# Optimization experiments

Hardware: AMD Instinct MI355X
Metric: run time of the kernel (lower is better)

Reference implementation:

```python
import jax, jax.numpy as jnp
import numpy as np

NUM_NODES = 32768  # B*N = 16*2048
NUM_REL = 10
NUM_BASES = 4
D = 256
E = 524288


def _rgcn_layer(x, src, dst, rel, basis, comp, root, bias):
    """Basis-decomposed relational GCN layer with per-relation mean aggregation.
    x: [N, Din], basis: [NB, Din, Dout], comp: [R, NB], root: [Din, Dout], bias: [Dout].
    """
    n = x.shape[0]
    # project all nodes through each basis once: [N, NB, Dout]
    xb = jnp.einsum('ni,bio->nbo', x, basis)
    coeff = comp[rel]  # [E, NB] per-edge basis coefficients
    # mean normalization per (destination node, relation) pair
    seg = rel * n + dst  # combined segment id, [E]
    cnt = jax.ops.segment_sum(jnp.ones(rel.shape[0], x.dtype), seg,
                              num_segments=NUM_REL * n)
    inv = jnp.where(cnt > 0, 1.0 / cnt, 0.0)[seg]  # [E]
    # per-edge message: sum_b coeff[e,b] * xb[src_e, b, :] (loop over small NB)
    msg = jnp.zeros((rel.shape[0], basis.shape[2]), x.dtype)
    for b in range(basis.shape[0]):
        msg = msg + coeff[:, b:b + 1] * xb[src, b]
    msg = msg * inv[:, None]
    agg = jax.ops.segment_sum(msg, dst, num_segments=n)  # [N, Dout]
    return agg + x @ root + bias


def setup_inputs() -> dict:
    key = jax.random.key(0)
    ks = jax.random.split(key, 16)
    p = lambda k, shp: (jax.random.normal(k, shp, jnp.float32) * 0.05)
    inp = {
        'x': jax.random.normal(ks[0], (16, 2048, D), jnp.float32),
        't': jax.random.randint(ks[1], (16,), 0, 1000),
        'obj_cond': jax.random.randint(ks[2], (16, 2048), 0, 160),
        'edge_cond': jax.random.randint(ks[3], (2, E), 0, NUM_NODES),
        'relation_cond': jax.random.randint(ks[4], (E,), 0, NUM_REL),
        # layer 0: 256 -> 256 (hidden)
        'basis0': p(ks[5], (NUM_BASES, D, D)),
        'comp0': p(ks[6], (NUM_REL, NUM_BASES)),
        'root0': p(ks[7], (D, D)),
        'bias0': p(ks[8], (D,)),
        # layer 1: 256 -> 256 (output)
        'basis1': p(ks[9], (NUM_BASES, D, D)),
        'comp1': p(ks[10], (NUM_REL, NUM_BASES)),
        'root1': p(ks[11], (D, D)),
        'bias1': p(ks[12], (D,)),
    }
    return inp


def reference(x, t, obj_cond, edge_cond, relation_cond,
              basis0, comp0, root0, bias0, basis1, comp1, root1, bias1):
    B, N, Dm = x.shape
    h = x.reshape(B * N, Dm)
    src, dst = edge_cond[0], edge_cond[1]
    h = _rgcn_layer(h, src, dst, relation_cond, basis0, comp0, root0, bias0)
    h = jax.nn.relu(h)  # hidden-layer activation (dropout disabled at eval)
    h = _rgcn_layer(h, src, dst, relation_cond, basis1, comp1, root1, bias1)
    return h.reshape(B, N, Dm)
```

## Files before the change

### kernel.cpp

```cpp
#include <hip/hip_runtime.h>
#include <stdint.h>

#define NNODES 32768
#define NREL 10
#define NBASES 4
#define DIM 256
#define NEDGE 524288
#define KW 1280
#define KBASE 1024

#define HB 2048
#define CB 8192
#define WB 80

typedef __attribute__((ext_vector_type(8))) short bf16x8;
typedef __attribute__((ext_vector_type(4))) float f32x4;

__device__ __forceinline__ float bf2f(unsigned short u){
  union { unsigned int i; float f; } v; v.i = ((unsigned int)u) << 16; return v.f;
}
__device__ __forceinline__ unsigned short f2bf(float f){
  union { float f; unsigned int i; } v; v.f = f;
  unsigned int x = v.i;
  unsigned int r = (x + 0x7FFFu + ((x >> 16) & 1u)) >> 16;
  return (unsigned short)r;
}
__device__ __forceinline__ void gll16(const void* g, void* l){
  __builtin_amdgcn_global_load_lds((const __attribute__((address_space(1))) void*)g,
                                   (__attribute__((address_space(3))) void*)l, 16, 0, 0);
}

__global__ __launch_bounds__(256) void mega_prep(
    const int* __restrict__ ec, const int* __restrict__ rel,
    int* __restrict__ cnt_rd,
    const float* __restrict__ x, unsigned short* __restrict__ Xh,
    const float* __restrict__ basis0, const float* __restrict__ root0,
    unsigned short* __restrict__ Wt0,
    const float* __restrict__ basis1, const float* __restrict__ root1,
    unsigned short* __restrict__ Wt1)
{
  __shared__ float tile[64][65];
  int bid = blockIdx.x;
  int t = threadIdx.x;
  if (bid < HB){
    int e = bid * 256 + t;
    int d = ec[NEDGE + e];
    int r = rel[e];
    atomicAdd(&cnt_rd[(r << 15) + d], 1);
  } else if (bid < HB + CB){
    int i = (bid - HB) * 256 + t;
    float4 v = ((const float4*)x)[i];
    ushort4 o; o.x = f2bf(v.x); o.y = f2bf(v.y); o.z = f2bf(v.z); o.w = f2bf(v.w);
    ((ushort4*)Xh)[i] = o;
  } else {
    int b = bid - HB - CB;
    int layer = b / WB; b %= WB;
    const float* basis = layer ? basis1 : basis0;
    const float* root  = layer ? root1  : root0;
    unsigned short* Wt = layer ? Wt1    : Wt0;
    int k0 = (b % 20) * 64;
    int n0 = (b / 20) * 64;
    int tn = t & 63, tk = t >> 6;
#pragma unroll
    for (int i = 0; i < 64; i += 4){
      int k = k0 + tk + i;
      float v = (k < KBASE) ? basis[(size_t)k * 256 + n0 + tn]
                            : root[(size_t)(k - KBASE) * 256 + n0 + tn];
      tile[tk + i][tn] = v;
    }
    __syncthreads();
#pragma unroll
    for (int i = 0; i < 64; i += 4){
      int n = n0 + tk + i;
      Wt[(size_t)n * KW + k0 + tn] = f2bf(tile[tn][tk + i]);
    }
  }
}

__global__ __launch_bounds__(1024) void scan1(const int* __restrict__ cnt_rd,
                                              int* __restrict__ offs, int* __restrict__ blksum)
{
  __shared__ int sh[1024];
  int tid = threadIdx.x; int gid = blockIdx.x * 1024 + tid;
  int v = 0;
#pragma unroll
  for (int r = 0; r < NREL; r++) v += cnt_rd[(r << 15) + gid];
  sh[tid] = v; __syncthreads();
  for (int off = 1; off < 1024; off <<= 1){
    int t = (tid >= off) ? sh[tid - off] : 0;
    __syncthreads(); sh[tid] += t; __syncthreads();
  }
  offs[gid] = sh[tid] - v;
  if (tid == 1023) blksum[blockIdx.x] = sh[1023];
}
__global__ __launch_bounds__(64) void scan2(int* __restrict__ blksum)
{
  __shared__ int sh[64];
  int tid = threadIdx.x;
  int v = (tid < NNODES / 1024) ? blksum[tid] : 0;
  sh[tid] = v; __syncthreads();
  for (int off = 1; off < 64; off <<= 1){
    int t = (tid >= off) ? sh[tid - off] : 0;
    __syncthreads(); sh[tid] += t; __syncthreads();
  }
  if (tid < NNODES / 1024) blksum[tid] = sh[tid] - v;
}
__global__ __launch_bounds__(1024) void scan3(int* __restrict__ offs, const int* __restrict__ blksum)
{
  int gid = blockIdx.x * 1024 + threadIdx.x;
  offs[gid] += blksum[blockIdx.x];
  if (gid == 0) offs[NNODES] = NEDGE;
}

__global__ void scatter_kernel(const int* __restrict__ ec, const int* __restrict__ rel,
                               const int* __restrict__ offs, int* __restrict__ cursor,
                               unsigned int* __restrict__ meta)
{
  int e = blockIdx.x * 256 + threadIdx.x;
  int s = ec[e];
  int d = ec[NEDGE + e];
  int r = rel[e];
  int p = offs[d] + atomicAdd(&cursor[d], 1);
  meta[p] = ((unsigned int)s << 4) | (unsigned int)r;
}

__global__ __launch_bounds__(256) void agg5(
    const unsigned short* __restrict__ Xin,
    const int* __restrict__ offs,
    const unsigned int* __restrict__ meta,
    const float* __restrict__ comp,
    const int* __restrict__ cnt_rd,
    unsigned short* __restrict__ z)
{
  __shared__ __attribute__((aligned(16))) float wtab[4][40];
  int t = threadIdx.x;
  int wv = t >> 6, lane = t & 63;
  int d = blockIdx.x * 4 + wv;
  if (lane < 40){
    int r = lane >> 2, b = lane & 3;
    int cnt = cnt_rd[(r << 15) + d];
    wtab[wv][lane] = (cnt > 0) ? comp[r * NBASES + b] / (float)cnt : 0.0f;
  }
  __syncthreads();

  int col = lane * 4;
  const float4* wt4 = (const float4*)&wtab[wv][0];

  float acc[NBASES][4] = {};
  int e0 = offs[d], e1 = offs[d + 1];
  int e = e0;
  for (; e + 3 < e1; e += 4){
    unsigned int m0 = meta[e], m1 = meta[e + 1], m2 = meta[e + 2], m3 = meta[e + 3];
    float4 w0 = wt4[m0 & 15u], w1 = wt4[m1 & 15u], w2 = wt4[m2 & 15u], w3 = wt4[m3 & 15u];
    ushort4 v0 = *(const ushort4*)(Xin + ((size_t)(m0 >> 4)) * 256 + col);
    ushort4 v1 = *(const ushort4*)(Xin + ((size_t)(m1 >> 4)) * 256 + col);
    ushort4 v2 = *(const ushort4*)(Xin + ((size_t)(m2 >> 4)) * 256 + col);
    ushort4 v3 = *(const ushort4*)(Xin + ((size_t)(m3 >> 4)) * 256 + col);
#pragma unroll
    for (int b = 0; b < NBASES; b++){
      float a0 = ((const float*)&w0)[b];
      float a1 = ((const float*)&w1)[b];
      float a2 = ((const float*)&w2)[b];
      float a3 = ((const float*)&w3)[b];
      acc[b][0] += a0 * bf2f(v0.x) + a1 * bf2f(v1.x) + a2 * bf2f(v2.x) + a3 * bf2f(v3.x);
      acc[b][1] += a0 * bf2f(v0.y) + a1 * bf2f(v1.y) + a2 * bf2f(v2.y) + a3 * bf2f(v3.y);
      acc[b][2] += a0 * bf2f(v0.z) + a1 * bf2f(v1.z) + a2 * bf2f(v2.z) + a3 * bf2f(v3.z);
      acc[b][3] += a0 * bf2f(v0.w) + a1 * bf2f(v1.w) + a2 * bf2f(v2.w) + a3 * bf2f(v3.w);
    }
  }
  for (; e < e1; ++e){
    unsigned int md = meta[e];
    float4 w = wt4[md & 15u];
    ushort4 v = *(const ushort4*)(Xin + ((size_t)(md >> 4)) * 256 + col);
#pragma unroll
    for (int b = 0; b < NBASES; b++){
      float a = ((const float*)&w)[b];
      acc[b][0] += a * bf2f(v.x); acc[b][1] += a * bf2f(v.y);
      acc[b][2] += a * bf2f(v.z); acc[b][3] += a * bf2f(v.w);
    }
  }
#pragma unroll
  for (int b = 0; b < NBASES; b++){
    ushort4 o;
    o.x = f2bf(acc[b][0]); o.y = f2bf(acc[b][1]);
    o.z = f2bf(acc[b][2]); o.w = f2bf(acc[b][3]);
    *(ushort4*)(z + (size_t)d * KBASE + b * 256 + col) = o;
  }
}

__global__ __launch_bounds__(256) void gemm4(
    const unsigned short* __restrict__ A0,
    const unsigned short* __restrict__ A1,
    const unsigned short* __restrict__ Wt,
    const float* __restrict__ bias,
    unsigned short* __restrict__ outh,
    float* __restrict__ outf,
    int mode)
{
  __shared__ __attribute__((aligned(16))) short As[64 * 32];
  __shared__ __attribute__((aligned(16))) short Bs[256 * 32];
  int tid  = threadIdx.x;
  int m0   = blockIdx.x * 64;
  int lane = tid & 63;
  int wn   = tid >> 6;
  int lq = lane >> 4, lr = lane & 15;

  f32x4 zero = {0.f, 0.f, 0.f, 0.f};
  f32x4 acc[4][4];
#pragma unroll
  for (int i = 0; i < 4; i++)
#pragma unroll
    for (int j = 0; j < 4; j++) acc[i][j] = zero;

  int arow = tid >> 2;
  int akc  = ((tid & 3) - (tid >> 3)) & 3;

  for (int k0 = 0; k0 < KW; k0 += 32){
    __syncthreads();
    {
      const unsigned short* ga;
      if (k0 < KBASE) ga = A0 + (size_t)(m0 + arow) * KBASE + k0 + akc * 8;
      else            ga = A1 + (size_t)(m0 + arow) * 256 + (k0 - KBASE) + akc * 8;
      gll16(ga, As + tid * 8);
    }
#pragma unroll
    for (int i = 0; i < 4; i++){
      int gb  = tid + i * 256;
      int row = gb >> 2;
      int kc  = ((gb & 3) - (gb >> 3)) & 3;
      gll16(Wt + (size_t)row * KW + k0 + kc * 8, Bs + gb * 8);
    }
    __syncthreads();

    bf16x8 af[4], bfr[4];
#pragma unroll
    for (int i = 0; i < 4; i++){
      int row = i * 16 + lr;
      af[i] = *(const bf16x8*)(As + row * 32 + (((lq + (row >> 1)) & 3) * 8));
    }
#pragma unroll
    for (int j = 0; j < 4; j++){
      int row = wn * 64 + j * 16 + lr;
      bfr[j] = *(const bf16x8*)(Bs + row * 32 + (((lq + (row >> 1)) & 3) * 8));
    }
#pragma unroll
    for (int i = 0; i < 4; i++)
#pragma unroll
      for (int j = 0; j < 4; j++)
        acc[i][j] = __builtin_amdgcn_mfma_f32_16x16x32_bf16(af[i], bfr[j], acc[i][j], 0, 0, 0);
  }

#pragma unroll
  for (int i = 0; i < 4; i++)
#pragma unroll
    for (int j = 0; j < 4; j++)
#pragma unroll
      for (int r = 0; r < 4; r++){
        int gm = m0 + i * 16 + lq * 4 + r;
        int gn = wn * 64 + j * 16 + lr;
        float v = acc[i][j][r] + bias[gn];
        size_t idx = (size_t)gm * 256 + gn;
        if (mode == 1) outh[idx] = f2bf(fmaxf(v, 0.f));
        else           outf[idx] = v;
      }
}

extern "C" void kernel_launch(void* const* d_in, const int* in_sizes, int n_in,
                              void* d_out, int out_size, void* d_ws, size_t ws_size,
                              hipStream_t stream)
{
  const float* x      = (const float*)d_in[0];
  const int*   ec     = (const int*)d_in[3];
  const int*   rel    = (const int*)d_in[4];
  const float* basis0 = (const float*)d_in[5];
  const float* comp0  = (const float*)d_in[6];
  const float* root0  = (const float*)d_in[7];
  const float* bias0  = (const float*)d_in[8];
  const float* basis1 = (const float*)d_in[9];
  const float* comp1  = (const float*)d_in[10];
  const float* root1  = (const float*)d_in[11];
  const float* bias1  = (const float*)d_in[12];

  char* p = (char*)d_ws;
  unsigned short* z   = (unsigned short*)p; p += (size_t)NNODES * KBASE * 2;
  unsigned short* Xh  = (unsigned short*)p; p += (size_t)NNODES * DIM * 2;
  unsigned short* h   = (unsigned short*)p; p += (size_t)NNODES * DIM * 2;
  unsigned short* Wt0 = (unsigned short*)p; p += (size_t)256 * KW * 2;
  unsigned short* Wt1 = (unsigned short*)p; p += (size_t)256 * KW * 2;
  unsigned int* meta  = (unsigned int*)p;   p += (size_t)NEDGE * 4;
  int* cnt_rd  = (int*)p;   p += (size_t)NREL * NNODES * 4;
  int* cursor  = (int*)p;   p += (size_t)NNODES * 4;
  int* offs    = (int*)p;   p += (size_t)(NNODES + 1) * 4;
  int* blksum  = (int*)p;   p += 1024;

  hipMemsetAsync(cnt_rd, 0, ((size_t)NREL * NNODES + (size_t)NNODES) * 4, stream);

  mega_prep<<<HB + CB + 2 * WB, 256, 0, stream>>>(
      ec, rel, cnt_rd, x, Xh, basis0, root0, Wt0, basis1, root1, Wt1);

  scan1<<<NNODES / 1024, 1024, 0, stream>>>(cnt_rd, offs, blksum);
  scan2<<<1, 64, 0, stream>>>(blksum);
  scan3<<<NNODES / 1024, 1024, 0, stream>>>(offs, blksum);
  scatter_kernel<<<NEDGE / 256, 256, 0, stream>>>(ec, rel, offs, cursor, meta);

  agg5<<<NNODES / 4, 256, 0, stream>>>(Xh, offs, meta, comp0, cnt_rd, z);
  gemm4<<<NNODES / 64, 256, 0, stream>>>(z, Xh, Wt0, bias0, h, nullptr, 1);

  agg5<<<NNODES / 4, 256, 0, stream>>>(h, offs, meta, comp1, cnt_rd, z);
  gemm4<<<NNODES / 64, 256, 0, stream>>>(z, h, Wt1, bias1, nullptr, (float*)d_out, 2);
}
```

Before: 331.0 us.

## Split each wavefront into two half-waves processing alternate edges with packed FMA

The aggregation kernel now has each half of a 64-lane wave handle a different edge. Each lane loads 8 bf16 values (16 bytes) instead of 4 and accumulates with packed two-wide float FMAs. The two halves' partial sums are combined with a cross-lane xor-32 shuffle, and each half writes two of the four basis outputs as 16-byte stores. This aims to widen the gather loads, halve the per-lane edge loop count and use packed math. The cost is a shuffle reduction, a masked tail for odd edge counts and more accumulator registers.

Measured after the change: 367.6 us. +11.0%, slower.

```diff
diff --git a/kernel.cpp b/kernel.cpp
--- a/kernel.cpp
+++ b/kernel.cpp
@@ -15,6 +15,8 @@
 
 typedef __attribute__((ext_vector_type(8))) short bf16x8;
 typedef __attribute__((ext_vector_type(4))) float f32x4;
+typedef __attribute__((ext_vector_type(2))) float f32x2;
+typedef __attribute__((ext_vector_type(8))) unsigned short u16x8;
 
 __device__ __forceinline__ float bf2f(unsigned short u){
   union { unsigned int i; float f; } v; v.i = ((unsigned int)u) << 16; return v.f;
@@ -124,7 +126,7 @@
   meta[p] = ((unsigned int)s << 4) | (unsigned int)r;
 }
 
-__global__ __launch_bounds__(256) void agg5(
+__global__ __launch_bounds__(256) void agg6(
     const unsigned short* __restrict__ Xin,
     const int* __restrict__ offs,
     const unsigned int* __restrict__ meta,
@@ -143,49 +145,82 @@
   }
   __syncthreads();
 
-  int col = lane * 4;
   const float4* wt4 = (const float4*)&wtab[wv][0];
-
-  float acc[NBASES][4] = {};
+  int h = lane >> 5;
+  unsigned cl8 = (unsigned)((lane & 31) * 8);
+
+  f32x2 acc[4][4];
+#pragma unroll
+  for (int b = 0; b < 4; b++)
+#pragma unroll
+    for (int j = 0; j < 4; j++) acc[b][j] = (f32x2){0.f, 0.f};
+
   int e0 = offs[d], e1 = offs[d + 1];
   int e = e0;
-  for (; e + 3 < e1; e += 4){
-    unsigned int m0 = meta[e], m1 = meta[e + 1], m2 = meta[e + 2], m3 = meta[e + 3];
-    float4 w0 = wt4[m0 & 15u], w1 = wt4[m1 & 15u], w2 = wt4[m2 & 15u], w3 = wt4[m3 & 15u];
-    ushort4 v0 = *(const ushort4*)(Xin + ((size_t)(m0 >> 4)) * 256 + col);
-    ushort4 v1 = *(const ushort4*)(Xin + ((size_t)(m1 >> 4)) * 256 + col);
-    ushort4 v2 = *(const ushort4*)(Xin + ((size_t)(m2 >> 4)) * 256 + col);
-    ushort4 v3 = *(const ushort4*)(Xin + ((size_t)(m3 >> 4)) * 256 + col);
-#pragma unroll
-    for (int b = 0; b < NBASES; b++){
-      float a0 = ((const float*)&w0)[b];
-      float a1 = ((const float*)&w1)[b];
-      float a2 = ((const float*)&w2)[b];
-      float a3 = ((const float*)&w3)[b];
-      acc[b][0] += a0 * bf2f(v0.x) + a1 * bf2f(v1.x) + a2 * bf2f(v2.x) + a3 * bf2f(v3.x);
-      acc[b][1] += a0 * bf2f(v0.y) + a1 * bf2f(v1.y) + a2 * bf2f(v2.y) + a3 * bf2f(v3.y);
-      acc[b][2] += a0 * bf2f(v0.z) + a1 * bf2f(v1.z) + a2 * bf2f(v2.z) + a3 * bf2f(v3.z);
-      acc[b][3] += a0 * bf2f(v0.w) + a1 * bf2f(v1.w) + a2 * bf2f(v2.w) + a3 * bf2f(v3.w);
-    }
-  }
-  for (; e < e1; ++e){
-    unsigned int md = meta[e];
-    float4 w = wt4[md & 15u];
-    ushort4 v = *(const ushort4*)(Xin + ((size_t)(md >> 4)) * 256 + col);
-#pragma unroll
-    for (int b = 0; b < NBASES; b++){
-      float a = ((const float*)&w)[b];
-      acc[b][0] += a * bf2f(v.x); acc[b][1] += a * bf2f(v.y);
-      acc[b][2] += a * bf2f(v.z); acc[b][3] += a * bf2f(v.w);
-    }
-  }
-#pragma unroll
-  for (int b = 0; b < NBASES; b++){
-    ushort4 o;
-    o.x = f2bf(acc[b][0]); o.y = f2bf(acc[b][1]);
-    o.z = f2bf(acc[b][2]); o.w = f2bf(acc[b][3]);
-    *(ushort4*)(z + (size_t)d * KBASE + b * 256 + col) = o;
-  }
+#pragma unroll 2
+  for (; e + 1 < e1; e += 2){
+    unsigned int m = meta[e + h];
+    float4 w4 = wt4[m & 15u];
+    f32x2 wd0 = {w4.x, w4.x}, wd1 = {w4.y, w4.y};
+    f32x2 wd2 = {w4.z, w4.z}, wd3 = {w4.w, w4.w};
+    union { uint4 q; unsigned int u[4]; } V;
+    V.q = *(const uint4*)(Xin + (unsigned)(m >> 4) * 256u + cl8);
+#pragma unroll
+    for (int j = 0; j < 4; j++){
+      unsigned int u = V.u[j];
+      union { unsigned int i; float f; } lo, hi;
+      lo.i = u << 16; hi.i = u & 0xffff0000u;
+      f32x2 vv = {lo.f, hi.f};
+      acc[0][j] += wd0 * vv;
+      acc[1][j] += wd1 * vv;
+      acc[2][j] += wd2 * vv;
+      acc[3][j] += wd3 * vv;
+    }
+  }
+  if (e < e1){
+    bool act = (h == 0);
+    unsigned int m = meta[act ? e : e0];
+    float4 w4 = wt4[m & 15u];
+    if (!act){ w4.x = 0.f; w4.y = 0.f; w4.z = 0.f; w4.w = 0.f; }
+    f32x2 wd0 = {w4.x, w4.x}, wd1 = {w4.y, w4.y};
+    f32x2 wd2 = {w4.z, w4.z}, wd3 = {w4.w, w4.w};
+    union { uint4 q; unsigned int u[4]; } V;
+    V.q = *(const uint4*)(Xin + (unsigned)(m >> 4) * 256u + cl8);
+#pragma unroll
+    for (int j = 0; j < 4; j++){
+      unsigned int u = V.u[j];
+      union { unsigned int i; float f; } lo, hi;
+      lo.i = u << 16; hi.i = u & 0xffff0000u;
+      f32x2 vv = {lo.f, hi.f};
+      acc[0][j] += wd0 * vv;
+      acc[1][j] += wd1 * vv;
+      acc[2][j] += wd2 * vv;
+      acc[3][j] += wd3 * vv;
+    }
+  }
+
+#pragma unroll
+  for (int b = 0; b < 4; b++)
+#pragma unroll
+    for (int j = 0; j < 4; j++){
+      acc[b][j].x += __shfl_xor(acc[b][j].x, 32);
+      acc[b][j].y += __shfl_xor(acc[b][j].y, 32);
+    }
+
+  u16x8 o0, o1;
+#pragma unroll
+  for (int j = 0; j < 4; j++){
+    f32x2 p = (h == 0) ? acc[0][j] : acc[2][j];
+    f32x2 q = (h == 0) ? acc[1][j] : acc[3][j];
+    o0[2 * j]     = f2bf(p.x);
+    o0[2 * j + 1] = f2bf(p.y);
+    o1[2 * j]     = f2bf(q.x);
+    o1[2 * j + 1] = f2bf(q.y);
+  }
+  size_t zb = (size_t)d * KBASE + cl8;
+  unsigned bofs = (unsigned)(h * 512);
+  *(u16x8*)(z + zb + bofs) = o0;
+  *(u16x8*)(z + zb + bofs + 256) = o1;
 }
 
 __global__ __launch_bounds__(256) void gemm4(
@@ -303,9 +338,9 @@
   scan3<<<NNODES / 1024, 1024, 0, stream>>>(offs, blksum);
   scatter_kernel<<<NEDGE / 256, 256, 0, stream>>>(ec, rel, offs, cursor, meta);
 
-  agg5<<<NNODES / 4, 256, 0, stream>>>(Xh, offs, meta, comp0, cnt_rd, z);
+  agg6<<<NNODES / 4, 256, 0, stream>>>(Xh, offs, meta, comp0, cnt_rd, z);
   gemm4<<<NNODES / 64, 256, 0, stream>>>(z, Xh, Wt0, bias0, h, nullptr, 1);
 
-  agg5<<<NNODES / 4, 256, 0, stream>>>(h, offs, meta, comp1, cnt_rd, z);
+  agg6<<<NNODES / 4, 256, 0, stream>>>(h, offs, meta, comp1, cnt_rd, z);
   gemm4<<<NNODES / 64, 256, 0, stream>>>(z, h, Wt1, bias1, nullptr, (float*)d_out, 2);
 }
```
